# Optimization experiments

Measured on AMD Instinct MI355X. Metric: run time of the kernel, lower is better.

The kernel has to match this reference:

```python
import jax, jax.numpy as jnp
import numpy as np

HIDDEN = 128
SIGMA_D = 0.2
SIGMA_A = 15.0
ANGLE_K = 10
FACTOR_A = 180.0 / (SIGMA_A * np.pi)


def _div_term():
    half = HIDDEN // 2
    return jnp.exp(jnp.arange(half, dtype=jnp.float32) * (-np.log(10000.0) / half))


def _sinusoid(x):
    # x: float tensor of (integer-valued) indices; returns x.shape + (HIDDEN,)
    pos = x[..., None].astype(jnp.float32)
    dt = _div_term()
    s = jnp.sin(pos * dt)
    c = jnp.cos(pos * dt)
    # interleave: even channels sin, odd channels cos
    return jnp.stack([s, c], axis=-1).reshape(x.shape + (HIDDEN,))


def setup_inputs() -> dict:
    key = jax.random.key(0)
    k1, k2, k3, k4, k5 = jax.random.split(key, 5)
    B, N = 2, 1024
    scale = 1.0 / np.sqrt(HIDDEN)
    points = jax.random.normal(k1, (B, N, 3), dtype=jnp.float32)
    Wd = jax.random.normal(k2, (HIDDEN, HIDDEN), dtype=jnp.float32) * scale
    bd = jax.random.normal(k3, (HIDDEN,), dtype=jnp.float32) * scale
    Wa = jax.random.normal(k4, (HIDDEN, HIDDEN), dtype=jnp.float32) * scale
    ba = jax.random.normal(k5, (HIDDEN,), dtype=jnp.float32) * scale
    return {"points": points, "Wd": Wd, "bd": bd, "Wa": Wa, "ba": ba}


def _single(pts, Wd, bd, Wa, ba):
    # pts: (N, 3)
    n = pts.shape[0]
    diff = pts[:, None, :] - pts[None, :, :]            # (N, N, 3)
    dists = jnp.sqrt(jnp.sum(diff * diff, axis=-1))      # (N, N)
    idx_d = jnp.clip(jnp.round(dists / SIGMA_D), 0.0, 255.0)
    # k nearest neighbours (smallest distances, incl. self)
    _, nn = jax.lax.top_k(-dists, ANGLE_K)               # (N, K)
    vec = pts[nn] - pts[:, None, :]                      # (N, K, 3)
    vnorm = jnp.linalg.norm(vec, axis=-1, keepdims=True)
    unit = vec / (vnorm + 1e-8)
    cos_ang = jnp.clip(jnp.einsum('nkd,nld->nkl', unit, unit), -1.0, 1.0)
    angles = jnp.arccos(cos_ang)                         # (N, K, K)
    idx_a = jnp.clip(jnp.round(angles * FACTOR_A), 0.0, 255.0)
    # indices computed under no_grad in the original
    idx_d = jax.lax.stop_gradient(idx_d)
    idx_a = jax.lax.stop_gradient(idx_a)

    embed_d = _sinusoid(idx_d)                           # (N, N, C)
    embed_d = jnp.mean(embed_d @ Wd.T + bd, axis=1)      # (N, C)

    embed_a = _sinusoid(idx_a)                           # (N, K, K, C)
    embed_a = embed_a @ Wa.T + ba
    embed_a = jnp.max(embed_a.reshape(n, -1, HIDDEN), axis=1)  # (N, C)
    return embed_d + embed_a


def reference(points, Wd, bd, Wa, ba):
    return jax.vmap(_single, in_axes=(0, None, None, None, None))(points, Wd, bd, Wa, ba)
```

## Files before the change

kernel.cpp:

```cpp
#include <hip/hip_runtime.h>
#include <hip/hip_bf16.h>

#define NPTS 1024
#define HID 128
#define KNN 10
#define PPB 2
#define FLT_MAX_ 3.402823466e+38f

__global__ __launch_bounds__(512) void gse_build(
    const float* __restrict__ Wd, const float* __restrict__ bd,
    const float* __restrict__ Wa, const float* __restrict__ ba,
    const float* __restrict__ pts, int nP,
    float* __restrict__ Td, float* __restrict__ Ta, float4* __restrict__ P4) {
    const int blk = blockIdx.x;
    const int tid = threadIdx.x;

    if (tid < 8) {
        for (int idx = blk * 8 + tid; idx < nP; idx += 272 * 8) {
            P4[idx] = make_float4(pts[idx * 3 + 0], pts[idx * 3 + 1],
                                  pts[idx * 3 + 2], 0.0f);
        }
    }

    __shared__ float S[HID];
    __shared__ float part[512];
    const bool isA = (blk >= 256);
    const int v = isA ? blk - 256 : blk;
    const int c = tid & 127;
    const int seg = tid >> 7;

    if (tid < HID) {
        const int m = tid >> 1;
        const float dtm = expf((float)m * (float)(-9.210340371976184 / 64.0));
        const float arg = (float)v * dtm;
        S[tid] = (tid & 1) ? cosf(arg) : sinf(arg);
    }
    __syncthreads();

    const float* W = isA ? Wa : Wd;
    const float* wrow = W + c * HID + seg * 32;
    const float* srow = S + seg * 32;
    float acc = 0.0f;
    #pragma unroll
    for (int h = 0; h < 32; h += 4) {
        const float4 wv = *reinterpret_cast<const float4*>(wrow + h);
        acc += srow[h] * wv.x + srow[h + 1] * wv.y + srow[h + 2] * wv.z + srow[h + 3] * wv.w;
    }
    part[tid] = acc;
    __syncthreads();

    if (tid < HID) {
        const float s = (part[c] + part[c + 128]) + (part[c + 256] + part[c + 384]);
        if (isA) Ta[v * HID + c] = s + ba[c];
        else     Td[v * HID + c] = (s + bd[c]) * (1.0f / (float)NPTS);
    }
}

__global__ __launch_bounds__(512, 8) void gse_main2(
    const float4* __restrict__ P4,
    const float* __restrict__ Td,
    const float* __restrict__ Ta,
    float* __restrict__ out) {
    const int tid = threadIdx.x;
    const int pt  = tid >> 8;
    const int t   = tid & 255;
    const int lane = tid & 63;
    const int w   = (tid >> 6) & 3;
    const int gid = blockIdx.x * PPB + pt;

    const int b = gid >> 10;
    const int i = gid & 1023;
    const float4* P = P4 + (size_t)b * NPTS;

    __shared__ int h4[PPB][4][256];
    __shared__ int hm[PPB][256];
    __shared__ unsigned long long cand[PPB][64];
    __shared__ int nn[PPB][KNN];
    __shared__ float sums[PPB][256], mxs[PPB][256];
    __shared__ unsigned amask_s[PPB];
    __shared__ int ccnt[PPB];
    __shared__ int meta_s[PPB];

    #pragma unroll
    for (int k = 0; k < 4; ++k) h4[pt][w][lane + k * 64] = 0;
    if (t == 0) { amask_s[pt] = 0u; ccnt[pt] = 0; }
    const float4 p = P[i];

    float d4[4];
    int q4[4];
    const int jb = w * 256;
    #pragma unroll
    for (int s = 0; s < 4; ++s) {
        const int j = jb + s * 64 + lane;
        const float4 q = P[j];
        const float dx = p.x - q.x;
        const float dy = p.y - q.y;
        const float dz = p.z - q.z;
        const float dd = sqrtf(dx * dx + dy * dy + dz * dz);
        d4[s] = dd;
        float qq = rintf(dd / 0.2f);
        qq = fminf(fmaxf(qq, 0.0f), 255.0f);
        q4[s] = (int)qq;
        atomicAdd(&h4[pt][w][q4[s]], 1);
    }
    __syncthreads();

    if (w == 0) {
        const int* H0 = h4[pt][0];
        const int* H1 = h4[pt][1];
        const int* H2 = h4[pt][2];
        const int* H3 = h4[pt][3];
        const int hv0 = H0[lane] + H1[lane] + H2[lane] + H3[lane];
        int cum = hv0;
        #pragma unroll
        for (int off = 1; off < 64; off <<= 1) {
            const int n_ = __shfl_up(cum, off);
            if (lane >= off) cum += n_;
        }
        const unsigned long long bal = __ballot(cum >= KNN);
        const int hv1 = H0[64 + lane] + H1[64 + lane] + H2[64 + lane] + H3[64 + lane];
        const int hv2 = H0[128 + lane] + H1[128 + lane] + H2[128 + lane] + H3[128 + lane];
        const int hv3 = H0[192 + lane] + H1[192 + lane] + H2[192 + lane] + H3[192 + lane];
        const unsigned long long nz0 = __ballot(hv0 != 0);
        const unsigned long long nz1 = __ballot(hv1 != 0);
        const unsigned long long nz2 = __ballot(hv2 != 0);
        const unsigned long long nz3 = __ballot(hv3 != 0);
        int maxbin;
        if (nz3)      maxbin = 192 + 63 - __clzll((long long)nz3);
        else if (nz2) maxbin = 128 + 63 - __clzll((long long)nz2);
        else if (nz1) maxbin = 64 + 63 - __clzll((long long)nz1);
        else          maxbin = 63 - __clzll((long long)nz0);
        int b10 = 0, c = 0;
        if (bal) { b10 = __ffsll(bal) - 1; c = __shfl(cum, b10); }
        const int fast = (bal != 0ull && c <= 64) ? 1 : 0;
        if (lane == 0) {
            meta_s[pt] = (b10 & 0xff) | ((fast ? c : 0) << 8)
                       | ((maxbin & 0xff) << 16) | (fast << 30);
        }
    } else if (w == 1) {
        #pragma unroll
        for (int k = 0; k < 2; ++k) {
            const int v = lane + k * 64;
            hm[pt][v] = h4[pt][0][v] + h4[pt][1][v] + h4[pt][2][v] + h4[pt][3][v];
        }
    } else if (w == 2) {
        #pragma unroll
        for (int k = 2; k < 4; ++k) {
            const int v = lane + k * 64;
            hm[pt][v] = h4[pt][0][v] + h4[pt][1][v] + h4[pt][2][v] + h4[pt][3][v];
        }
    }
    __syncthreads();
    const int meta = meta_s[pt];
    const int b10 = meta & 0xff;
    const int c = (meta >> 8) & 0xff;
    const int maxbin = (meta >> 16) & 0xff;
    const bool fast = ((meta >> 30) & 1) != 0;

    if (fast) {
        #pragma unroll
        for (int s = 0; s < 4; ++s) {
            const bool pred = (q4[s] <= b10);
            const unsigned long long m = __ballot(pred);
            if (m) {
                int base = 0;
                if (lane == 0) base = atomicAdd(&ccnt[pt], __popcll(m));
                base = __shfl(base, 0);
                if (pred) {
                    const int pos = base + (int)__popcll(m & ((1ull << lane) - 1ull));
                    const int idx = jb + s * 64 + lane;
                    cand[pt][pos] = ((unsigned long long)__float_as_uint(d4[s]) << 32)
                                  | (unsigned)idx;
                }
            }
        }
    } else {
        unsigned valid = 0xfu;
        unsigned long long keep = 0;
        for (int r = 0; r < KNN; ++r) {
            float bv = FLT_MAX_;
            int bi = 0x7fffffff;
            #pragma unroll
            for (int s = 0; s < 4; ++s) {
                if (valid & (1u << s)) {
                    const float v_ = d4[s];
                    const int id_ = jb + s * 64 + lane;
                    if (v_ < bv || (v_ == bv && id_ < bi)) { bv = v_; bi = id_; }
                }
            }
            #pragma unroll
            for (int off = 32; off > 0; off >>= 1) {
                const float ov = __shfl_xor(bv, off);
                const int oi = __shfl_xor(bi, off);
                if (ov < bv || (ov == bv && oi < bi)) { bv = ov; bi = oi; }
            }
            const int loc = bi - jb;
            if (loc >= 0 && loc < 256 && lane == (loc & 63)) valid &= ~(1u << (loc >> 6));
            if (lane == r) keep = ((unsigned long long)__float_as_uint(bv) << 32)
                                | (unsigned)bi;
        }
        if (lane < KNN) cand[pt][w * KNN + lane] = keep;
    }
    __syncthreads();

    const int ncand = fast ? c : 4 * KNN;
    if (t < ncand) {
        const unsigned long long my = cand[pt][t];
        int rank = 0;
        #pragma unroll 8
        for (int pp = 0; pp < ncand; ++pp) {
            rank += (cand[pt][pp] < my) ? 1 : 0;
        }
        if (rank < KNN) nn[pt][rank] = (int)(my & 0xffffffffu);
    }
    __syncthreads();

    if (t < KNN * KNN) {
        const int k = t / KNN, l = t % KNN;
        const int jk = nn[pt][k], jl = nn[pt][l];
        const float4 qk = P[jk];
        const float4 ql = P[jl];
        const float kx = qk.x - p.x;
        const float ky = qk.y - p.y;
        const float kz = qk.z - p.z;
        const float dk = sqrtf(kx * kx + ky * ky + kz * kz) + 1e-8f;
        const float lx = ql.x - p.x;
        const float ly = ql.y - p.y;
        const float lz = ql.z - p.z;
        const float dl = sqrtf(lx * lx + ly * ly + lz * lz) + 1e-8f;
        float cc = (kx / dk) * (lx / dl) + (ky / dk) * (ly / dl) + (kz / dk) * (lz / dl);
        cc = fminf(fmaxf(cc, -1.0f), 1.0f);
        const float ang = acosf(cc);
        float q = rintf(ang * (float)(180.0 / (15.0 * M_PI)));
        q = fminf(fmaxf(q, 0.0f), 15.0f);
        atomicOr(&amask_s[pt], 1u << (int)q);
    }
    __syncthreads();

    const unsigned am = amask_s[pt];
    const int c7 = t & 127;
    const int half = t >> 7;
    float s = 0.0f;
    const float* tdc = Td + c7;
    #pragma unroll 4
    for (int v = half; v <= maxbin; v += 2) {
        s += (float)hm[pt][v] * tdc[v * HID];
    }
    float mx = -FLT_MAX_;
    const float* tac = Ta + c7;
    #pragma unroll
    for (int v = 0; v < 8; ++v) {
        const int vv = half * 8 + v;
        const float tv = tac[vv * HID];
        if (am & (1u << vv)) mx = fmaxf(mx, tv);
    }
    sums[pt][t] = s;
    mxs[pt][t] = mx;
    __syncthreads();
    if (t < HID) {
        out[(size_t)gid * HID + t] =
            (sums[pt][t] + sums[pt][t + 128]) + fmaxf(mxs[pt][t], mxs[pt][t + 128]);
    }
}

__global__ __launch_bounds__(256, 8) void gse_main(
    const float4* __restrict__ P4,
    const float* __restrict__ Td,
    const float* __restrict__ Ta,
    float* __restrict__ out) {
    const int gid = blockIdx.x;
    const int b = gid >> 10;
    const int i = gid & 1023;
    const float4* P = P4 + (size_t)b * NPTS;
    const int tid = threadIdx.x;
    const int lane = tid & 63;
    const int w = tid >> 6;

    __shared__ int h4[4][256];
    __shared__ unsigned long long cand[64];
    __shared__ int nn[KNN];
    __shared__ float sums[256], mxs[256];
    __shared__ unsigned amask_s;
    __shared__ int ccnt;
    __shared__ int meta_s;

    {
        int* hf = (int*)h4;
        hf[tid] = 0; hf[tid + 256] = 0; hf[tid + 512] = 0; hf[tid + 768] = 0;
    }
    if (tid == 0) { amask_s = 0u; ccnt = 0; }
    const float4 p = P[i];
    __syncthreads();

    float d4[4];
    int q4[4];
    const int jb = w * 256;
    #pragma unroll
    for (int s = 0; s < 4; ++s) {
        const int j = jb + s * 64 + lane;
        const float4 q = P[j];
        const float dx = p.x - q.x;
        const float dy = p.y - q.y;
        const float dz = p.z - q.z;
        const float dd = sqrtf(dx * dx + dy * dy + dz * dz);
        d4[s] = dd;
        float qq = rintf(dd / 0.2f);
        qq = fminf(fmaxf(qq, 0.0f), 255.0f);
        q4[s] = (int)qq;
        atomicAdd(&h4[w][q4[s]], 1);
    }
    __syncthreads();

    const int hsum = h4[0][tid] + h4[1][tid] + h4[2][tid] + h4[3][tid];
    h4[0][tid] = hsum;
    __syncthreads();
    const int* hist = h4[0];

    if (w == 0) {
        int cum = hist[lane];
        #pragma unroll
        for (int off = 1; off < 64; off <<= 1) {
            const int n_ = __shfl_up(cum, off);
            if (lane >= off) cum += n_;
        }
        const unsigned long long bal = __ballot(cum >= KNN);
        const unsigned long long nz0 = __ballot(hist[lane] != 0);
        const unsigned long long nz1 = __ballot(hist[64 + lane] != 0);
        const unsigned long long nz2 = __ballot(hist[128 + lane] != 0);
        const unsigned long long nz3 = __ballot(hist[192 + lane] != 0);
        int maxbin;
        if (nz3)      maxbin = 192 + 63 - __clzll((long long)nz3);
        else if (nz2) maxbin = 128 + 63 - __clzll((long long)nz2);
        else if (nz1) maxbin = 64 + 63 - __clzll((long long)nz1);
        else          maxbin = 63 - __clzll((long long)nz0);
        int b10 = 0, c = 0;
        if (bal) { b10 = __ffsll(bal) - 1; c = __shfl(cum, b10); }
        const int fast = (bal != 0ull && c <= 64) ? 1 : 0;
        if (lane == 0) {
            meta_s = (b10 & 0xff) | ((fast ? c : 0) << 8)
                   | ((maxbin & 0xff) << 16) | (fast << 30);
        }
    }
    __syncthreads();
    const int meta = meta_s;
    const int b10 = meta & 0xff;
    const int c = (meta >> 8) & 0xff;
    const int maxbin = (meta >> 16) & 0xff;
    const bool fast = ((meta >> 30) & 1) != 0;

    if (fast) {
        #pragma unroll
        for (int s = 0; s < 4; ++s) {
            const bool pred = (q4[s] <= b10);
            const unsigned long long m = __ballot(pred);
            if (m) {
                int base = 0;
                if (lane == 0) base = atomicAdd(&ccnt, __popcll(m));
                base = __shfl(base, 0);
                if (pred) {
                    const int pos = base + (int)__popcll(m & ((1ull << lane) - 1ull));
                    const int idx = jb + s * 64 + lane;
                    cand[pos] = ((unsigned long long)__float_as_uint(d4[s]) << 32)
                              | (unsigned)idx;
                }
            }
        }
        __syncthreads();
        if (tid < c) {
            const unsigned long long my = cand[tid];
            int rank = 0;
            #pragma unroll 8
            for (int pp = 0; pp < c; ++pp) rank += (cand[pp] < my) ? 1 : 0;
            if (rank < KNN) nn[rank] = (int)(my & 0xffffffffu);
        }
        __syncthreads();
    } else {
        unsigned valid = 0xfu;
        unsigned long long keep = 0;
        for (int r = 0; r < KNN; ++r) {
            float bv = FLT_MAX_;
            int bi = 0x7fffffff;
            #pragma unroll
            for (int s = 0; s < 4; ++s) {
                if (valid & (1u << s)) {
                    const float v_ = d4[s];
                    const int id_ = jb + s * 64 + lane;
                    if (v_ < bv || (v_ == bv && id_ < bi)) { bv = v_; bi = id_; }
                }
            }
            #pragma unroll
            for (int off = 32; off > 0; off >>= 1) {
                const float ov = __shfl_xor(bv, off);
                const int oi = __shfl_xor(bi, off);
                if (ov < bv || (ov == bv && oi < bi)) { bv = ov; bi = oi; }
            }
            const int loc = bi - jb;
            if (loc >= 0 && loc < 256 && lane == (loc & 63)) valid &= ~(1u << (loc >> 6));
            if (lane == r) keep = ((unsigned long long)__float_as_uint(bv) << 32)
                                | (unsigned)bi;
        }
        if (lane < KNN) cand[w * KNN + lane] = keep;
        __syncthreads();
        if (tid < 4 * KNN) {
            const unsigned long long my = cand[tid];
            int rank = 0;
            for (int pp = 0; pp < 4 * KNN; ++pp) rank += (cand[pp] < my) ? 1 : 0;
            if (rank < KNN) nn[rank] = (int)(my & 0xffffffffu);
        }
        __syncthreads();
    }

    if (tid < KNN * KNN) {
        const int k = tid / KNN, l = tid % KNN;
        const int jk = nn[k], jl = nn[l];
        const float4 qk = P[jk];
        const float4 ql = P[jl];
        const float kx = qk.x - p.x;
        const float ky = qk.y - p.y;
        const float kz = qk.z - p.z;
        const float dk = sqrtf(kx * kx + ky * ky + kz * kz) + 1e-8f;
        const float lx = ql.x - p.x;
        const float ly = ql.y - p.y;
        const float lz = ql.z - p.z;
        const float dl = sqrtf(lx * lx + ly * ly + lz * lz) + 1e-8f;
        float cc = (kx / dk) * (lx / dl) + (ky / dk) * (ly / dl) + (kz / dk) * (lz / dl);
        cc = fminf(fmaxf(cc, -1.0f), 1.0f);
        const float ang = acosf(cc);
        float q = rintf(ang * (float)(180.0 / (15.0 * M_PI)));
        q = fminf(fmaxf(q, 0.0f), 15.0f);
        atomicOr(&amask_s, 1u << (int)q);
    }
    __syncthreads();

    const unsigned am = amask_s;
    const int c7 = tid & 127;
    const int half = tid >> 7;
    float s = 0.0f;
    const float* tdc = Td + c7;
    #pragma unroll 4
    for (int v = half; v <= maxbin; v += 2) {
        s += (float)hist[v] * tdc[v * HID];
    }
    float mx = -FLT_MAX_;
    const float* tac = Ta + c7;
    #pragma unroll
    for (int v = 0; v < 8; ++v) {
        const int vv = half * 8 + v;
        const float tv = tac[vv * HID];
        if (am & (1u << vv)) mx = fmaxf(mx, tv);
    }
    sums[tid] = s;
    mxs[tid] = mx;
    __syncthreads();
    if (tid < HID) {
        out[(size_t)gid * HID + tid] =
            (sums[tid] + sums[tid + 128]) + fmaxf(mxs[tid], mxs[tid + 128]);
    }
}

extern "C" void kernel_launch(void* const* d_in, const int* in_sizes, int n_in,
                              void* d_out, int out_size, void* d_ws, size_t ws_size,
                              hipStream_t stream) {
    const float* pts = (const float*)d_in[0];
    const float* Wd  = (const float*)d_in[1];
    const float* bd  = (const float*)d_in[2];
    const float* Wa  = (const float*)d_in[3];
    const float* ba  = (const float*)d_in[4];
    float* out = (float*)d_out;

    const int B = in_sizes[0] / (NPTS * 3);
    const int nP = B * NPTS;

    float* Td = (float*)d_ws;
    float* Ta = Td + 256 * HID;
    float4* P4 = (float4*)(Ta + 16 * HID);

    gse_build<<<272, 512, 0, stream>>>(Wd, bd, Wa, ba, pts, nP, Td, Ta, P4);
    if (nP % PPB == 0) {
        gse_main2<<<nP / PPB, PPB * 256, 0, stream>>>(P4, Td, Ta, out);
    } else {
        gse_main<<<nP, 256, 0, stream>>>(P4, Td, Ta, out);
    }
}
```

Measured before the change: 20.38 us.

## Overlap histogram-table dot product with kNN rank selection across waves

While wave 0 ranks the kNN candidates, waves 1-3 now compute the distance-histogram times Td dot product using float2 loads, storing partial sums in shared memory. The final epilogue runs on wave 0 alone: it combines the three partials, takes the masked angle max over Ta with float2 loads, and writes the output directly. This removes one barrier and the separate 256-thread reduction stage, at the cost of leaving waves idle in the epilogue and splitting the histogram loop over only three waves.

```diff
diff --git a/kernel.cpp b/kernel.cpp
--- a/kernel.cpp
+++ b/kernel.cpp
@@ -76,7 +76,7 @@
     __shared__ int hm[PPB][256];
     __shared__ unsigned long long cand[PPB][64];
     __shared__ int nn[PPB][KNN];
-    __shared__ float sums[PPB][256], mxs[PPB][256];
+    __shared__ float2 pdot[PPB][3][64];
     __shared__ unsigned amask_s[PPB];
     __shared__ int ccnt[PPB];
     __shared__ int meta_s[PPB];
@@ -204,14 +204,27 @@
     __syncthreads();
 
     const int ncand = fast ? c : 4 * KNN;
-    if (t < ncand) {
-        const unsigned long long my = cand[pt][t];
-        int rank = 0;
-        #pragma unroll 8
-        for (int pp = 0; pp < ncand; ++pp) {
-            rank += (cand[pt][pp] < my) ? 1 : 0;
-        }
-        if (rank < KNN) nn[pt][rank] = (int)(my & 0xffffffffu);
+    if (w == 0) {
+        if (t < ncand) {
+            const unsigned long long my = cand[pt][t];
+            int rank = 0;
+            #pragma unroll 8
+            for (int pp = 0; pp < ncand; ++pp) {
+                rank += (cand[pt][pp] < my) ? 1 : 0;
+            }
+            if (rank < KNN) nn[pt][rank] = (int)(my & 0xffffffffu);
+        }
+    } else {
+        const int k3 = w - 1;
+        const float2* td2 = reinterpret_cast<const float2*>(Td);
+        float sx = 0.0f, sy = 0.0f;
+        for (int v = k3; v <= maxbin; v += 3) {
+            const float h = (float)hm[pt][v];
+            const float2 tv = td2[(size_t)v * 64 + lane];
+            sx += h * tv.x;
+            sy += h * tv.y;
+        }
+        pdot[pt][k3][lane] = make_float2(sx, sy);
     }
     __syncthreads();
 
@@ -237,29 +250,22 @@
     }
     __syncthreads();
 
-    const unsigned am = amask_s[pt];
-    const int c7 = t & 127;
-    const int half = t >> 7;
-    float s = 0.0f;
-    const float* tdc = Td + c7;
-    #pragma unroll 4
-    for (int v = half; v <= maxbin; v += 2) {
-        s += (float)hm[pt][v] * tdc[v * HID];
-    }
-    float mx = -FLT_MAX_;
-    const float* tac = Ta + c7;
-    #pragma unroll
-    for (int v = 0; v < 8; ++v) {
-        const int vv = half * 8 + v;
-        const float tv = tac[vv * HID];
-        if (am & (1u << vv)) mx = fmaxf(mx, tv);
-    }
-    sums[pt][t] = s;
-    mxs[pt][t] = mx;
-    __syncthreads();
-    if (t < HID) {
-        out[(size_t)gid * HID + t] =
-            (sums[pt][t] + sums[pt][t + 128]) + fmaxf(mxs[pt][t], mxs[pt][t + 128]);
+    if (w == 0) {
+        const unsigned am = amask_s[pt];
+        const float2 a0 = pdot[pt][0][lane];
+        const float2 a1 = pdot[pt][1][lane];
+        const float2 a2 = pdot[pt][2][lane];
+        float sx = (a0.x + a1.x) + a2.x;
+        float sy = (a0.y + a1.y) + a2.y;
+        const float2* ta2 = reinterpret_cast<const float2*>(Ta);
+        float mxx = -FLT_MAX_, mxy = -FLT_MAX_;
+        #pragma unroll
+        for (int v = 0; v < 16; ++v) {
+            const float2 tv = ta2[v * 64 + lane];
+            if (am & (1u << v)) { mxx = fmaxf(mxx, tv.x); mxy = fmaxf(mxy, tv.y); }
+        }
+        float2* o2 = reinterpret_cast<float2*>(out + (size_t)gid * HID);
+        o2[lane] = make_float2(sx + mxx, sy + mxy);
     }
 }
 
```

Result: slower. 21.52 us (+5.6%).
